# Kernel optimization log

Hardware: AMD Instinct MI355X
Metric: run time of the kernel (lower is better)

The kernel has to match this reference:

```python
import jax, jax.numpy as jnp
import numpy as np

N_NODES = 10000
N_EDGES = 320000
IN_DIM = 512
HID = 64
H0 = 8
OUT = 64
H1 = 1
NEG_SLOPE = 0.2


def gat_layer(h, src, dst, W, attn_l, attn_r, n_nodes, activation=None):
    # h: (N, F_in); W: (F_in, H*D); attn_l/attn_r: (H, D)
    H, D = attn_l.shape
    feat = (h @ W).reshape(n_nodes, H, D)            # (N, H, D)
    el = jnp.einsum('nhd,hd->nh', feat, attn_l)      # (N, H)
    er = jnp.einsum('nhd,hd->nh', feat, attn_r)      # (N, H)
    e = jax.nn.leaky_relu(el[src] + er[dst], NEG_SLOPE)  # (E, H)
    # edge softmax over incoming edges of each destination node
    m = jax.ops.segment_max(e, dst, num_segments=n_nodes)   # (N, H), -inf for isolated
    m = jnp.where(jnp.isfinite(m), m, 0.0)
    ex = jnp.exp(e - m[dst])                         # (E, H)
    s = jax.ops.segment_sum(ex, dst, num_segments=n_nodes)  # (N, H)
    alpha = ex / s[dst]                              # (E, H)
    # weighted aggregation: out[dst] += alpha * feat[src]
    out = jax.ops.segment_sum(alpha[:, :, None] * feat[src], dst,
                              num_segments=n_nodes)  # (N, H, D)
    if activation is not None:
        out = activation(out)
    return out


def setup_inputs() -> dict:
    key = jax.random.key(0)
    ks = jax.random.split(key, 9)
    h = jax.random.normal(ks[0], (N_NODES, IN_DIM), dtype=jnp.float32)
    src = jax.random.randint(ks[1], (N_EDGES,), 0, N_NODES, dtype=jnp.int32)
    dst = jax.random.randint(ks[2], (N_EDGES,), 0, N_NODES, dtype=jnp.int32)
    W1 = jax.random.normal(ks[3], (IN_DIM, H0 * HID), dtype=jnp.float32) / np.sqrt(IN_DIM)
    attn_l1 = jax.random.normal(ks[4], (H0, HID), dtype=jnp.float32) / np.sqrt(HID)
    attn_r1 = jax.random.normal(ks[5], (H0, HID), dtype=jnp.float32) / np.sqrt(HID)
    W2 = jax.random.normal(ks[6], (H0 * HID, H1 * OUT), dtype=jnp.float32) / np.sqrt(H0 * HID)
    attn_l2 = jax.random.normal(ks[7], (H1, OUT), dtype=jnp.float32) / np.sqrt(OUT)
    attn_r2 = jax.random.normal(ks[8], (H1, OUT), dtype=jnp.float32) / np.sqrt(OUT)
    return {"h": h, "src": src, "dst": dst, "W1": W1, "attn_l1": attn_l1,
            "attn_r1": attn_r1, "W2": W2, "attn_l2": attn_l2, "attn_r2": attn_r2}


def reference(h, src, dst, W1, attn_l1, attn_r1, W2, attn_l2, attn_r2):
    # layer 1: elu activation, concat heads (flatten)
    x = gat_layer(h, src, dst, W1, attn_l1, attn_r1, N_NODES, activation=jax.nn.elu)
    x = x.reshape(N_NODES, H0 * HID)
    # layer 2: no activation, mean over heads
    x = gat_layer(x, src, dst, W2, attn_l2, attn_r2, N_NODES, activation=None)
    return x.mean(axis=1)  # (N, OUT)
```

## Files before the change

kernel.cpp:

```cpp
#include <hip/hip_runtime.h>
#include <hip/hip_bf16.h>
#include <math.h>

typedef unsigned int u32;
typedef unsigned short ushort;

constexpr int N_NODES = 10000;
constexpr int N_EDGES = 320000;
constexpr float NEG_SLOPE = 0.2f;

typedef __attribute__((ext_vector_type(8))) short short8;
typedef __attribute__((ext_vector_type(4))) float f32x4;
typedef __attribute__((ext_vector_type(16))) float f32x16;

__device__ __forceinline__ float lrelu(float x) { return x > 0.f ? x : NEG_SLOPE * x; }
__device__ __forceinline__ float elu(float x)   { return x > 0.f ? x : (expf(x) - 1.f); }

__device__ __forceinline__ ushort f2bf(float x) {
    u32 b = __float_as_uint(x);
    b += 0x7FFFu + ((b >> 16) & 1u);
    return (ushort)(b >> 16);
}
__device__ __forceinline__ float bf2f(ushort u) {
    return __uint_as_float(((u32)u) << 16);
}

__device__ __forceinline__ void gload16(const void* g, void* l) {
    __builtin_amdgcn_global_load_lds(
        (__attribute__((address_space(1))) void*)g,
        (__attribute__((address_space(3))) void*)l, 16, 0, 0);
}

constexpr int NBZ_CNT = (N_NODES + 255) / 256;
__global__ void zero_kernel(int* __restrict__ counts,
                            const float* __restrict__ W2,
                            const float* __restrict__ al2, const float* __restrict__ ar2,
                            float* __restrict__ wl2, float* __restrict__ wr2) {
    const int b = blockIdx.x;
    if (b < NBZ_CNT) {
        const int j = b * 256 + threadIdx.x;
        if (j < N_NODES) counts[j] = 0;
    } else {
        const int k = (b - NBZ_CNT) * 256 + threadIdx.x;
        float sl = 0.f, sr = 0.f;
#pragma unroll 8
        for (int d = 0; d < 64; d++) {
            const float w = W2[(size_t)k * 64 + d];
            sl += w * al2[d];
            sr += w * ar2[d];
        }
        wl2[k] = sl;
        wr2[k] = sr;
    }
}

constexpr int NB_SPLIT = (N_NODES * 512 / 4) / 256;
constexpr int NB_T1    = 64;
constexpr int NB_T2    = 8;
constexpr int NB_HIST  = (N_EDGES + 255) / 256;

__global__ void prep_kernel(const float4* __restrict__ h4,
                            ushort* __restrict__ hhi, ushort* __restrict__ hlo,
                            const float* __restrict__ W1,
                            ushort* __restrict__ w1thi, ushort* __restrict__ w1tlo,
                            const float* __restrict__ W2,
                            ushort* __restrict__ w2thi,
                            const int* __restrict__ dst, int* __restrict__ counts,
                            int* __restrict__ rank) {
    __shared__ float smem[64][65];
    const int b = blockIdx.x;
    if (b < NB_HIST) {
        const int i = b * 256 + threadIdx.x;
        if (i < N_EDGES) rank[i] = atomicAdd(&counts[dst[i]], 1);
    } else if (b < NB_HIST + NB_SPLIT) {
        const int i = (b - NB_HIST) * 256 + threadIdx.x;
        const float4 v = h4[i];
        ushort h0 = f2bf(v.x), h1 = f2bf(v.y), h2 = f2bf(v.z), h3 = f2bf(v.w);
        *(ushort4*)&hhi[i * 4] = make_ushort4(h0, h1, h2, h3);
        *(ushort4*)&hlo[i * 4] = make_ushort4(
            f2bf(v.x - bf2f(h0)), f2bf(v.y - bf2f(h1)),
            f2bf(v.z - bf2f(h2)), f2bf(v.w - bf2f(h3)));
    } else {
        const bool isW1 = b < NB_HIST + NB_SPLIT + NB_T1;
        const float* W = isW1 ? W1 : W2;
        const int N  = isW1 ? 512 : 64;
        const int t  = isW1 ? (b - NB_HIST - NB_SPLIT) : (b - NB_HIST - NB_SPLIT - NB_T1);
        const int ti = isW1 ? (t & 7) : t;
        const int tj = isW1 ? (t >> 3) : 0;
        const int c  = threadIdx.x & 63;
        const int r0 = threadIdx.x >> 6;
#pragma unroll
        for (int p = 0; p < 16; p++) {
            const int r = p * 4 + r0;
            smem[r][c] = W[(size_t)(ti * 64 + r) * N + tj * 64 + c];
        }
        __syncthreads();
        if (isW1) {
#pragma unroll
            for (int p = 0; p < 16; p++) {
                const int rr = p * 4 + r0;
                const float v = smem[c][rr];
                const ushort hh = f2bf(v);
                w1thi[(size_t)(tj * 64 + rr) * 512 + ti * 64 + c] = hh;
                w1tlo[(size_t)(tj * 64 + rr) * 512 + ti * 64 + c] = f2bf(v - bf2f(hh));
            }
        } else {
#pragma unroll
            for (int p = 0; p < 16; p++) {
                const int rr = p * 4 + r0;
                w2thi[(size_t)(tj * 64 + rr) * 512 + ti * 64 + c] = f2bf(smem[c][rr]);
            }
        }
    }
}

__global__ __launch_bounds__(1024) void scan_kernel(
    const int* __restrict__ counts, int* __restrict__ offs, int n) {
    __shared__ int wsum[16];
    const int tid = threadIdx.x;
    const int lane = tid & 63, wave = tid >> 6;
    const int base = tid * 10;
    int v[10];
    int s = 0;
#pragma unroll
    for (int i = 0; i < 10; i++) {
        v[i] = (base + i < n) ? counts[base + i] : 0;
        s += v[i];
    }
    int ps = s;
#pragma unroll
    for (int o = 1; o < 64; o <<= 1) {
        const int t = __shfl_up(ps, o);
        if (lane >= o) ps += t;
    }
    if (lane == 63) wsum[wave] = ps;
    __syncthreads();
    if (tid < 16) {
        int t = wsum[tid];
#pragma unroll
        for (int o = 1; o < 16; o <<= 1) {
            const int u = __shfl_up(t, o);
            if (tid >= o) t += u;
        }
        wsum[tid] = t;
    }
    __syncthreads();
    const int wbase = (wave > 0) ? wsum[wave - 1] : 0;
    int run = wbase + ps - s;
#pragma unroll
    for (int i = 0; i < 10; i++) {
        if (base + i < n) offs[base + i + 1] = run + v[i];
        run += v[i];
    }
    if (tid == 0) offs[0] = 0;
}

constexpr int NB_GEMM1 = ((N_NODES + 63) / 64) * 4;
constexpr int NB_SCAT  = (N_EDGES + 255) / 256;

__global__ __launch_bounds__(256) void gemm1_scatter_kernel(
    const ushort* __restrict__ Ahi, const ushort* __restrict__ Alo,
    const ushort* __restrict__ Bhi, const ushort* __restrict__ Blo,
    ushort* __restrict__ Cout, int M,
    const float* __restrict__ attn_l, const float* __restrict__ attn_r,
    float* __restrict__ elp, float* __restrict__ erp,
    const int* __restrict__ src, const int* __restrict__ dst,
    const int* __restrict__ rank, const int* __restrict__ offs,
    int* __restrict__ srcs) {
    constexpr int BM = 64, BN = 128, BK = 32, K = 512, N = 512;

    if ((int)blockIdx.x >= NB_GEMM1) {
        const int i = ((int)blockIdx.x - NB_GEMM1) * 256 + threadIdx.x;
        if (i < N_EDGES) srcs[offs[dst[i]] + rank[i]] = src[i];
        return;
    }

    __shared__ __align__(16) ushort sAhi[BM * BK];
    __shared__ __align__(16) ushort sAlo[BM * BK];
    __shared__ __align__(16) ushort sBhi[BN * BK];
    __shared__ __align__(16) ushort sBlo[BN * BK];

    const int tid = threadIdx.x;
    const int wave = tid >> 6, lane = tid & 63;
    const int m0 = ((int)blockIdx.x >> 2) * BM, n0 = ((int)blockIdx.x & 3) * BN;
    const int wm = wave >> 1, wn = wave & 1;
    const int l31 = lane & 31, lh = lane >> 5;

    const int fb = wave * 1024 + lane * 16;

    int arow = m0 + (fb >> 6);
    if (arow > M - 1) arow = M - 1;
    const size_t abyte = (size_t)arow * (K * 2) + (fb & 63);
    size_t bbyte[2];
#pragma unroll
    for (int r = 0; r < 2; r++) {
        const int f = fb + r * 4096;
        bbyte[r] = (size_t)(n0 + (f >> 6)) * (K * 2) + (f & 63);
    }

    f32x16 acc[2] = {};

    for (int k0 = 0; k0 < K; k0 += BK) {
        __syncthreads();
        const size_t kb = (size_t)k0 * 2;
        gload16((const char*)Ahi + abyte + kb, (char*)sAhi + fb);
        gload16((const char*)Alo + abyte + kb, (char*)sAlo + fb);
#pragma unroll
        for (int r = 0; r < 2; r++) {
            const int f = fb + r * 4096;
            gload16((const char*)Bhi + bbyte[r] + kb, (char*)sBhi + f);
            gload16((const char*)Blo + bbyte[r] + kb, (char*)sBlo + f);
        }
        __syncthreads();

#pragma unroll
        for (int ks = 0; ks < 2; ks++) {
            const int koff = ks * 16 + lh * 8;
            const int arw = wm * 32 + l31;
            const short8 ah = *(const short8*)&sAhi[arw * BK + koff];
            const short8 al = *(const short8*)&sAlo[arw * BK + koff];
            short8 bh[2], bl[2];
#pragma unroll
            for (int ni = 0; ni < 2; ni++) {
                const int brw = wn * 64 + ni * 32 + l31;
                bh[ni] = *(const short8*)&sBhi[brw * BK + koff];
                bl[ni] = *(const short8*)&sBlo[brw * BK + koff];
            }
#pragma unroll
            for (int ni = 0; ni < 2; ni++) {
                acc[ni] = __builtin_amdgcn_mfma_f32_32x32x16_bf16(ah, bh[ni], acc[ni], 0, 0, 0);
                acc[ni] = __builtin_amdgcn_mfma_f32_32x32x16_bf16(ah, bl[ni], acc[ni], 0, 0, 0);
                acc[ni] = __builtin_amdgcn_mfma_f32_32x32x16_bf16(al, bh[ni], acc[ni], 0, 0, 0);
            }
        }
    }

#pragma unroll
    for (int reg = 0; reg < 16; reg++) {
        const int grow = m0 + wm * 32 + (reg & 3) + 8 * (reg >> 2) + 4 * lh;
        if (grow < M) {
#pragma unroll
            for (int ni = 0; ni < 2; ni++) {
                const int gcol = n0 + wn * 64 + ni * 32 + l31;
                Cout[(size_t)grow * N + gcol] = f2bf(acc[ni][reg]);
            }
        }
    }

    const int head = (n0 + wn * 64) >> 6;
    float alv[2], arv[2];
#pragma unroll
    for (int ni = 0; ni < 2; ni++) {
        alv[ni] = attn_l[head * 64 + ni * 32 + l31];
        arv[ni] = attn_r[head * 64 + ni * 32 + l31];
    }
#pragma unroll
    for (int reg = 0; reg < 16; reg++) {
        float pl = acc[0][reg] * alv[0] + acc[1][reg] * alv[1];
        float pr = acc[0][reg] * arv[0] + acc[1][reg] * arv[1];
#pragma unroll
        for (int o = 1; o < 32; o <<= 1) {
            pl += __shfl_xor(pl, o);
            pr += __shfl_xor(pr, o);
        }
        const int grow = m0 + wm * 32 + (reg & 3) + 8 * (reg >> 2) + 4 * lh;
        if (l31 == 0 && grow < M) {
            elp[grow * 8 + head] = pl;
            erp[grow * 8 + head] = pr;
        }
    }
}

__global__ __launch_bounds__(256) void gemm2_kernel(
    const ushort* __restrict__ Ahi, const ushort* __restrict__ Bhi,
    float* __restrict__ Cout, int M) {
    constexpr int BM = 64, BN = 64, BK = 32, K = 512, N = 64;
    constexpr int WM = 32, WN = 32, MT_M = 2, MT_N = 2;

    __shared__ __align__(16) ushort sA[BM * BK];
    __shared__ __align__(16) ushort sB[BN * BK];

    const int tid = threadIdx.x;
    const int wave = tid >> 6, lane = tid & 63;
    const int m0 = blockIdx.x * BM;
    const int wm = wave >> 1, wn = wave & 1;
    const int quad = lane >> 4, l15 = lane & 15;

    const int fb = wave * 1024 + lane * 16;

    int arow = m0 + (fb >> 6);
    if (arow > M - 1) arow = M - 1;
    const size_t abyte = (size_t)arow * (K * 2) + (fb & 63);
    const size_t bbyte = (size_t)(fb >> 6) * (K * 2) + (fb & 63);

    f32x4 acc[MT_M][MT_N] = {};

    for (int k0 = 0; k0 < K; k0 += BK) {
        __syncthreads();
        const size_t kb = (size_t)k0 * 2;
        gload16((const char*)Ahi + abyte + kb, (char*)sA + fb);
        gload16((const char*)Bhi + bbyte + kb, (char*)sB + fb);
        __syncthreads();

        short8 ah[MT_M], bh[MT_N];
#pragma unroll
        for (int mi = 0; mi < MT_M; mi++) {
            const int row = wm * WM + mi * 16 + l15;
            ah[mi] = *(const short8*)&sA[row * BK + quad * 8];
        }
#pragma unroll
        for (int ni = 0; ni < MT_N; ni++) {
            const int row = wn * WN + ni * 16 + l15;
            bh[ni] = *(const short8*)&sB[row * BK + quad * 8];
        }
#pragma unroll
        for (int mi = 0; mi < MT_M; mi++)
#pragma unroll
            for (int ni = 0; ni < MT_N; ni++)
                acc[mi][ni] = __builtin_amdgcn_mfma_f32_16x16x32_bf16(ah[mi], bh[ni], acc[mi][ni], 0, 0, 0);
    }

#pragma unroll
    for (int mi = 0; mi < MT_M; mi++) {
#pragma unroll
        for (int r = 0; r < 4; r++) {
            const int grow = m0 + wm * WM + mi * 16 + quad * 4 + r;
            if (grow < M) {
#pragma unroll
                for (int ni = 0; ni < MT_N; ni++) {
                    const int gcol = wn * WN + ni * 16 + l15;
                    Cout[(size_t)grow * N + gcol] = acc[mi][ni][r];
                }
            }
        }
    }
}

__global__ __launch_bounds__(256) void agg1_kernel(
    const ushort* __restrict__ feat, const float* __restrict__ el,
    const float* __restrict__ er, const int* __restrict__ offs,
    const int* __restrict__ srcs, ushort* __restrict__ xhi,
    const float* __restrict__ wl2, const float* __restrict__ wr2,
    float* __restrict__ el2, float* __restrict__ er2) {
    const int tid = threadIdx.x;
    const int wave = tid >> 6, lane = tid & 63;
    const int node = blockIdx.x * 4 + wave;
    const int start = offs[node];
    const int deg = offs[node + 1] - start;
    const int d0 = lane * 8;
    const int myh = lane >> 3;

    if (deg == 0) {
        const ushort4 z = make_ushort4(0, 0, 0, 0);
        *(ushort4*)&xhi[(size_t)node * 512 + d0] = z;
        *(ushort4*)&xhi[(size_t)node * 512 + d0 + 4] = z;
        if (lane == 0) { el2[node] = 0.f; er2[node] = 0.f; }
        return;
    }

    const float4 ea = *(const float4*)&er[node * 8];
    const float4 eb = *(const float4*)&er[node * 8 + 4];
    const float er_my = (myh & 4) ? ((myh & 2) ? ((myh & 1) ? eb.w : eb.z)
                                              : ((myh & 1) ? eb.y : eb.x))
                                  : ((myh & 2) ? ((myh & 1) ? ea.w : ea.z)
                                              : ((myh & 1) ? ea.y : ea.x));

    float acc[8];
#pragma unroll
    for (int i = 0; i < 8; i++) acc[i] = 0.f;
    float ws = 0.f;

    for (int base = 0; base < deg; base += 64) {
        const int has = min(64, deg - base);
        const int s = srcs[start + base + min(lane, has - 1)];
        int j = 0;
        for (; j + 8 <= has; j += 8) {
            int sq[8];
#pragma unroll
            for (int q = 0; q < 8; q++) sq[q] = __shfl(s, j + q);
            float eq[8];
#pragma unroll
            for (int q = 0; q < 8; q++) eq[q] = el[sq[q] * 8 + myh];
            short8 uq[8];
#pragma unroll
            for (int q = 0; q < 8; q++)
                uq[q] = *(const short8*)&feat[(size_t)sq[q] * 512 + d0];
            float wq[8];
#pragma unroll
            for (int q = 0; q < 8; q++) wq[q] = __expf(lrelu(eq[q] + er_my));
#pragma unroll
            for (int q = 0; q < 8; q++) {
#pragma unroll
                for (int i = 0; i < 8; i++)
                    acc[i] += wq[q] * bf2f((ushort)uq[q][i]);
                ws += wq[q];
            }
        }
        for (; j < has; j++) {
            const int sj = __shfl(s, j);
            const float w = __expf(lrelu(el[sj * 8 + myh] + er_my));
            const short8 u = *(const short8*)&feat[(size_t)sj * 512 + d0];
#pragma unroll
            for (int i = 0; i < 8; i++)
                acc[i] += w * bf2f((ushort)u[i]);
            ws += w;
        }
    }

    const float inv = 1.f / ws;
    float o[8];
#pragma unroll
    for (int i = 0; i < 8; i++) o[i] = elu(acc[i] * inv);

    const float4 wla = *(const float4*)&wl2[d0];
    const float4 wlb = *(const float4*)&wl2[d0 + 4];
    const float4 wra = *(const float4*)&wr2[d0];
    const float4 wrb = *(const float4*)&wr2[d0 + 4];
    float pl = o[0] * wla.x + o[1] * wla.y + o[2] * wla.z + o[3] * wla.w
             + o[4] * wlb.x + o[5] * wlb.y + o[6] * wlb.z + o[7] * wlb.w;
    float pr = o[0] * wra.x + o[1] * wra.y + o[2] * wra.z + o[3] * wra.w
             + o[4] * wrb.x + o[5] * wrb.y + o[6] * wrb.z + o[7] * wrb.w;
#pragma unroll
    for (int off = 32; off > 0; off >>= 1) {
        pl += __shfl_xor(pl, off);
        pr += __shfl_xor(pr, off);
    }
    if (lane == 0) { el2[node] = pl; er2[node] = pr; }

    ushort hi[8];
#pragma unroll
    for (int i = 0; i < 8; i++) hi[i] = f2bf(o[i]);
    *(ushort4*)&xhi[(size_t)node * 512 + d0]     = make_ushort4(hi[0], hi[1], hi[2], hi[3]);
    *(ushort4*)&xhi[(size_t)node * 512 + d0 + 4] = make_ushort4(hi[4], hi[5], hi[6], hi[7]);
}

__global__ __launch_bounds__(256) void agg2_kernel(
    const float* __restrict__ feat, const float* __restrict__ el,
    const float* __restrict__ er, const int* __restrict__ offs,
    const int* __restrict__ srcs, float* __restrict__ out) {
    const int tid = threadIdx.x;
    const int wave = tid >> 6, lane = tid & 63;
    const int node = blockIdx.x * 4 + wave;
    const int start = offs[node];
    const int deg = offs[node + 1] - start;
    if (deg == 0) { out[(size_t)node * 64 + lane] = 0.f; return; }
    const float ern = er[node];

    float acc = 0.f, ws = 0.f;
    for (int base = 0; base < deg; base += 64) {
        const int has = min(64, deg - base);
        const int s = srcs[start + base + min(lane, has - 1)];
        const float w = __expf(lrelu(el[s] + ern));
        int j = 0;
        for (; j + 8 <= has; j += 8) {
            float aq[8]; int sq[8];
#pragma unroll
            for (int q = 0; q < 8; q++) { aq[q] = __shfl(w, j + q); sq[q] = __shfl(s, j + q); }
            float fq[8];
#pragma unroll
            for (int q = 0; q < 8; q++) fq[q] = feat[(size_t)sq[q] * 64 + lane];
#pragma unroll
            for (int q = 0; q < 8; q++) { acc += aq[q] * fq[q]; ws += aq[q]; }
        }
        for (; j < has; j++) {
            const float a = __shfl(w, j);
            const int sj = __shfl(s, j);
            acc += a * feat[(size_t)sj * 64 + lane];
            ws += a;
        }
    }
    out[(size_t)node * 64 + lane] = acc / ws;
}

extern "C" void kernel_launch(void* const* d_in, const int* in_sizes, int n_in,
                              void* d_out, int out_size, void* d_ws, size_t ws_size,
                              hipStream_t stream) {
    const float* h   = (const float*)d_in[0];
    const int*   src = (const int*)d_in[1];
    const int*   dst = (const int*)d_in[2];
    const float* W1  = (const float*)d_in[3];
    const float* al1 = (const float*)d_in[4];
    const float* ar1 = (const float*)d_in[5];
    const float* W2  = (const float*)d_in[6];
    const float* al2 = (const float*)d_in[7];
    const float* ar2 = (const float*)d_in[8];
    float* out = (float*)d_out;

    char* p = (char*)d_ws;
    ushort* feat1bf = (ushort*)p; p += (size_t)N_NODES * 512 * 2;
    float* feat2 = (float*)p;  p += (size_t)N_NODES * 64 * 4;
    float* el1   = (float*)p;  p += (size_t)N_NODES * 8 * 4;
    float* er1   = (float*)p;  p += (size_t)N_NODES * 8 * 4;
    float* el2   = (float*)p;  p += (size_t)N_NODES * 4;
    float* er2   = (float*)p;  p += (size_t)N_NODES * 4;
    ushort* xhi  = (ushort*)p; p += (size_t)N_NODES * 512 * 2;
    ushort* xlo  = (ushort*)p; p += (size_t)N_NODES * 512 * 2;
    ushort* w1thi = (ushort*)p; p += (size_t)512 * 512 * 2;
    ushort* w1tlo = (ushort*)p; p += (size_t)512 * 512 * 2;
    ushort* w2thi = (ushort*)p; p += (size_t)64 * 512 * 2;
    float* wl2   = (float*)p;  p += (size_t)512 * 4;
    float* wr2   = (float*)p;  p += (size_t)512 * 4;
    int* counts  = (int*)p;    p += (size_t)N_NODES * 4;
    int* offs    = (int*)p;    p += (size_t)10004 * 4;
    int* rank    = (int*)p;    p += (size_t)N_EDGES * 4;
    int* srcs    = (int*)p;    p += (size_t)N_EDGES * 4;

    zero_kernel<<<NBZ_CNT + 2, 256, 0, stream>>>(counts, W2, al2, ar2, wl2, wr2);

    prep_kernel<<<NB_HIST + NB_SPLIT + NB_T1 + NB_T2, 256, 0, stream>>>(
        (const float4*)h, xhi, xlo, W1, w1thi, w1tlo, W2, w2thi,
        dst, counts, rank);

    scan_kernel<<<1, 1024, 0, stream>>>(counts, offs, N_NODES);

    gemm1_scatter_kernel<<<NB_GEMM1 + NB_SCAT, 256, 0, stream>>>(
        xhi, xlo, w1thi, w1tlo, feat1bf, N_NODES, al1, ar1, el1, er1,
        src, dst, rank, offs, srcs);

    agg1_kernel<<<N_NODES / 4, 256, 0, stream>>>(
        feat1bf, el1, er1, offs, srcs, xhi, wl2, wr2, el2, er2);

    gemm2_kernel<<<(N_NODES + 63) / 64, 256, 0, stream>>>(
        xhi, w2thi, feat2, N_NODES);

    agg2_kernel<<<N_NODES / 4, 256, 0, stream>>>(feat2, el2, er2, offs, srcs, out);
}
```

Baseline: 209.5 us.

## Fold scan into weight-prep kernel, memset counts, store layer-2 features as bf16

Replaces the zero kernel with a memset, moves the W1/W2 transposes and the wl2/wr2 projection out of the histogram/split kernel into a second prep kernel, and folds the prefix scan into that kernel as a single 256-thread block. This cuts one launch and lets the weight transposes run alongside the scan. Layer-2 GEMM output is also stored as bf16 instead of fp32, halving gather traffic in agg2 at some precision cost. The scan now runs in one 256-thread block with 40 elements per thread, which is serial work on a single block.

Measured after the change: 210.4 us. About the same (+0.4%).

```diff
diff --git a/kernel.cpp b/kernel.cpp
--- a/kernel.cpp
+++ b/kernel.cpp
@@ -31,48 +31,18 @@
         (__attribute__((address_space(3))) void*)l, 16, 0, 0);
 }
 
-constexpr int NBZ_CNT = (N_NODES + 255) / 256;
-__global__ void zero_kernel(int* __restrict__ counts,
-                            const float* __restrict__ W2,
-                            const float* __restrict__ al2, const float* __restrict__ ar2,
-                            float* __restrict__ wl2, float* __restrict__ wr2) {
-    const int b = blockIdx.x;
-    if (b < NBZ_CNT) {
-        const int j = b * 256 + threadIdx.x;
-        if (j < N_NODES) counts[j] = 0;
-    } else {
-        const int k = (b - NBZ_CNT) * 256 + threadIdx.x;
-        float sl = 0.f, sr = 0.f;
-#pragma unroll 8
-        for (int d = 0; d < 64; d++) {
-            const float w = W2[(size_t)k * 64 + d];
-            sl += w * al2[d];
-            sr += w * ar2[d];
-        }
-        wl2[k] = sl;
-        wr2[k] = sr;
-    }
-}
-
+constexpr int NB_HIST  = (N_EDGES + 255) / 256;
 constexpr int NB_SPLIT = (N_NODES * 512 / 4) / 256;
-constexpr int NB_T1    = 64;
-constexpr int NB_T2    = 8;
-constexpr int NB_HIST  = (N_EDGES + 255) / 256;
-
-__global__ void prep_kernel(const float4* __restrict__ h4,
-                            ushort* __restrict__ hhi, ushort* __restrict__ hlo,
-                            const float* __restrict__ W1,
-                            ushort* __restrict__ w1thi, ushort* __restrict__ w1tlo,
-                            const float* __restrict__ W2,
-                            ushort* __restrict__ w2thi,
-                            const int* __restrict__ dst, int* __restrict__ counts,
-                            int* __restrict__ rank) {
-    __shared__ float smem[64][65];
+
+__global__ void prep1_kernel(const float4* __restrict__ h4,
+                             ushort* __restrict__ hhi, ushort* __restrict__ hlo,
+                             const int* __restrict__ dst, int* __restrict__ counts,
+                             int* __restrict__ rank) {
     const int b = blockIdx.x;
     if (b < NB_HIST) {
         const int i = b * 256 + threadIdx.x;
         if (i < N_EDGES) rank[i] = atomicAdd(&counts[dst[i]], 1);
-    } else if (b < NB_HIST + NB_SPLIT) {
+    } else {
         const int i = (b - NB_HIST) * 256 + threadIdx.x;
         const float4 v = h4[i];
         ushort h0 = f2bf(v.x), h1 = f2bf(v.y), h2 = f2bf(v.z), h3 = f2bf(v.w);
@@ -80,11 +50,27 @@
         *(ushort4*)&hlo[i * 4] = make_ushort4(
             f2bf(v.x - bf2f(h0)), f2bf(v.y - bf2f(h1)),
             f2bf(v.z - bf2f(h2)), f2bf(v.w - bf2f(h3)));
-    } else {
-        const bool isW1 = b < NB_HIST + NB_SPLIT + NB_T1;
+    }
+}
+
+constexpr int NB_T1   = 64;
+constexpr int NB_T2   = 8;
+constexpr int NB_WLR2 = 2;
+
+__global__ void prep2_kernel(const float* __restrict__ W1,
+                             ushort* __restrict__ w1thi, ushort* __restrict__ w1tlo,
+                             const float* __restrict__ W2,
+                             ushort* __restrict__ w2thi,
+                             const float* __restrict__ al2, const float* __restrict__ ar2,
+                             float* __restrict__ wl2, float* __restrict__ wr2,
+                             const int* __restrict__ counts, int* __restrict__ offs) {
+    __shared__ float smem[64][65];
+    const int b = blockIdx.x;
+    if (b < NB_T1 + NB_T2) {
+        const bool isW1 = b < NB_T1;
         const float* W = isW1 ? W1 : W2;
         const int N  = isW1 ? 512 : 64;
-        const int t  = isW1 ? (b - NB_HIST - NB_SPLIT) : (b - NB_HIST - NB_SPLIT - NB_T1);
+        const int t  = isW1 ? b : (b - NB_T1);
         const int ti = isW1 ? (t & 7) : t;
         const int tj = isW1 ? (t >> 3) : 0;
         const int c  = threadIdx.x & 63;
@@ -111,48 +97,56 @@
                 w2thi[(size_t)(tj * 64 + rr) * 512 + ti * 64 + c] = f2bf(smem[c][rr]);
             }
         }
-    }
-}
-
-__global__ __launch_bounds__(1024) void scan_kernel(
-    const int* __restrict__ counts, int* __restrict__ offs, int n) {
-    __shared__ int wsum[16];
-    const int tid = threadIdx.x;
-    const int lane = tid & 63, wave = tid >> 6;
-    const int base = tid * 10;
-    int v[10];
-    int s = 0;
-#pragma unroll
-    for (int i = 0; i < 10; i++) {
-        v[i] = (base + i < n) ? counts[base + i] : 0;
-        s += v[i];
-    }
-    int ps = s;
-#pragma unroll
-    for (int o = 1; o < 64; o <<= 1) {
-        const int t = __shfl_up(ps, o);
-        if (lane >= o) ps += t;
-    }
-    if (lane == 63) wsum[wave] = ps;
-    __syncthreads();
-    if (tid < 16) {
-        int t = wsum[tid];
-#pragma unroll
-        for (int o = 1; o < 16; o <<= 1) {
-            const int u = __shfl_up(t, o);
-            if (tid >= o) t += u;
-        }
-        wsum[tid] = t;
-    }
-    __syncthreads();
-    const int wbase = (wave > 0) ? wsum[wave - 1] : 0;
-    int run = wbase + ps - s;
-#pragma unroll
-    for (int i = 0; i < 10; i++) {
-        if (base + i < n) offs[base + i + 1] = run + v[i];
-        run += v[i];
-    }
-    if (tid == 0) offs[0] = 0;
+    } else if (b < NB_T1 + NB_T2 + NB_WLR2) {
+        const int k = (b - NB_T1 - NB_T2) * 256 + threadIdx.x;
+        float sl = 0.f, sr = 0.f;
+#pragma unroll 8
+        for (int d = 0; d < 64; d++) {
+            const float w = W2[(size_t)k * 64 + d];
+            sl += w * al2[d];
+            sr += w * ar2[d];
+        }
+        wl2[k] = sl;
+        wr2[k] = sr;
+    } else {
+        __shared__ int wsum[4];
+        const int tid = threadIdx.x;
+        const int lane = tid & 63, wave = tid >> 6;
+        const int base = tid * 40;
+        int v[40];
+        int s = 0;
+#pragma unroll
+        for (int i = 0; i < 40; i++) {
+            v[i] = (base + i < N_NODES) ? counts[base + i] : 0;
+            s += v[i];
+        }
+        int ps = s;
+#pragma unroll
+        for (int o = 1; o < 64; o <<= 1) {
+            const int t = __shfl_up(ps, o);
+            if (lane >= o) ps += t;
+        }
+        if (lane == 63) wsum[wave] = ps;
+        __syncthreads();
+        if (tid < 4) {
+            int t = wsum[tid];
+#pragma unroll
+            for (int o = 1; o < 4; o <<= 1) {
+                const int u = __shfl_up(t, o);
+                if (tid >= o) t += u;
+            }
+            wsum[tid] = t;
+        }
+        __syncthreads();
+        const int wbase = (wave > 0) ? wsum[wave - 1] : 0;
+        int run = wbase + ps - s;
+#pragma unroll
+        for (int i = 0; i < 40; i++) {
+            if (base + i < N_NODES) offs[base + i + 1] = run + v[i];
+            run += v[i];
+        }
+        if (tid == 0) offs[0] = 0;
+    }
 }
 
 constexpr int NB_GEMM1 = ((N_NODES + 63) / 64) * 4;
@@ -273,7 +267,7 @@
 
 __global__ __launch_bounds__(256) void gemm2_kernel(
     const ushort* __restrict__ Ahi, const ushort* __restrict__ Bhi,
-    float* __restrict__ Cout, int M) {
+    ushort* __restrict__ Cout, int M) {
     constexpr int BM = 64, BN = 64, BK = 32, K = 512, N = 64;
     constexpr int WM = 32, WN = 32, MT_M = 2, MT_N = 2;
 
@@ -329,7 +323,7 @@
 #pragma unroll
                 for (int ni = 0; ni < MT_N; ni++) {
                     const int gcol = wn * WN + ni * 16 + l15;
-                    Cout[(size_t)grow * N + gcol] = acc[mi][ni][r];
+                    Cout[(size_t)grow * N + gcol] = f2bf(acc[mi][ni][r]);
                 }
             }
         }
@@ -435,7 +429,7 @@
 }
 
 __global__ __launch_bounds__(256) void agg2_kernel(
-    const float* __restrict__ feat, const float* __restrict__ el,
+    const ushort* __restrict__ feat, const float* __restrict__ el,
     const float* __restrict__ er, const int* __restrict__ offs,
     const int* __restrict__ srcs, float* __restrict__ out) {
     const int tid = threadIdx.x;
@@ -456,16 +450,16 @@
             float aq[8]; int sq[8];
 #pragma unroll
             for (int q = 0; q < 8; q++) { aq[q] = __shfl(w, j + q); sq[q] = __shfl(s, j + q); }
-            float fq[8];
+            ushort fq[8];
 #pragma unroll
             for (int q = 0; q < 8; q++) fq[q] = feat[(size_t)sq[q] * 64 + lane];
 #pragma unroll
-            for (int q = 0; q < 8; q++) { acc += aq[q] * fq[q]; ws += aq[q]; }
+            for (int q = 0; q < 8; q++) { acc += aq[q] * bf2f(fq[q]); ws += aq[q]; }
         }
         for (; j < has; j++) {
             const float a = __shfl(w, j);
             const int sj = __shfl(s, j);
-            acc += a * feat[(size_t)sj * 64 + lane];
+            acc += a * bf2f(feat[(size_t)sj * 64 + lane]);
             ws += a;
         }
     }
@@ -488,7 +482,7 @@
 
     char* p = (char*)d_ws;
     ushort* feat1bf = (ushort*)p; p += (size_t)N_NODES * 512 * 2;
-    float* feat2 = (float*)p;  p += (size_t)N_NODES * 64 * 4;
+    ushort* feat2bf = (ushort*)p; p += (size_t)N_NODES * 64 * 2;
     float* el1   = (float*)p;  p += (size_t)N_NODES * 8 * 4;
     float* er1   = (float*)p;  p += (size_t)N_NODES * 8 * 4;
     float* el2   = (float*)p;  p += (size_t)N_NODES * 4;
@@ -505,13 +499,13 @@
     int* rank    = (int*)p;    p += (size_t)N_EDGES * 4;
     int* srcs    = (int*)p;    p += (size_t)N_EDGES * 4;
 
-    zero_kernel<<<NBZ_CNT + 2, 256, 0, stream>>>(counts, W2, al2, ar2, wl2, wr2);
-
-    prep_kernel<<<NB_HIST + NB_SPLIT + NB_T1 + NB_T2, 256, 0, stream>>>(
-        (const float4*)h, xhi, xlo, W1, w1thi, w1tlo, W2, w2thi,
-        dst, counts, rank);
-
-    scan_kernel<<<1, 1024, 0, stream>>>(counts, offs, N_NODES);
+    hipMemsetAsync(counts, 0, (size_t)N_NODES * 4, stream);
+
+    prep1_kernel<<<NB_HIST + NB_SPLIT, 256, 0, stream>>>(
+        (const float4*)h, xhi, xlo, dst, counts, rank);
+
+    prep2_kernel<<<NB_T1 + NB_T2 + NB_WLR2 + 1, 256, 0, stream>>>(
+        W1, w1thi, w1tlo, W2, w2thi, al2, ar2, wl2, wr2, counts, offs);
 
     gemm1_scatter_kernel<<<NB_GEMM1 + NB_SCAT, 256, 0, stream>>>(
         xhi, xlo, w1thi, w1tlo, feat1bf, N_NODES, al1, ar1, el1, er1,
@@ -521,7 +515,7 @@
         feat1bf, el1, er1, offs, srcs, xhi, wl2, wr2, el2, er2);
 
     gemm2_kernel<<<(N_NODES + 63) / 64, 256, 0, stream>>>(
-        xhi, w2thi, feat2, N_NODES);
-
-    agg2_kernel<<<N_NODES / 4, 256, 0, stream>>>(feat2, el2, er2, offs, srcs, out);
-}
+        xhi, w2thi, feat2bf, N_NODES);
+
+    agg2_kernel<<<N_NODES / 4, 256, 0, stream>>>(feat2bf, el2, er2, offs, srcs, out);
+}
```
